# Performance work log

Measured on AMD Instinct MI355X. Metric: run time of the kernel, lower is better.

## Reference

```python
import jax, jax.numpy as jnp
import numpy as np
from math import sqrt

B, T, C, H = 4, 2048, 1024, 16
D = C // H  # head dim = 64


def setup_inputs() -> dict:
    key = jax.random.key(0)
    ks = jax.random.split(key, 9)
    s = 1.0 / sqrt(C)
    return {
        "x": jax.random.normal(ks[0], (B, T, C), dtype=jnp.float32),
        "Wk": jax.random.normal(ks[1], (C, C), dtype=jnp.float32) * s,
        "bk": jax.random.normal(ks[2], (C,), dtype=jnp.float32) * 0.01,
        "Wq": jax.random.normal(ks[3], (C, C), dtype=jnp.float32) * s,
        "bq": jax.random.normal(ks[4], (C,), dtype=jnp.float32) * 0.01,
        "Wv": jax.random.normal(ks[5], (C, C), dtype=jnp.float32) * s,
        "bv": jax.random.normal(ks[6], (C,), dtype=jnp.float32) * 0.01,
        "Wp": jax.random.normal(ks[7], (C, C), dtype=jnp.float32) * s,
        "bp": jax.random.normal(ks[8], (C,), dtype=jnp.float32) * 0.01,
    }


def reference(x, Wk, bk, Wq, bq, Wv, bv, Wp, bp):
    # Linear projections, split into heads: [B, H, T, D]
    def heads(y):
        return y.reshape(B, T, H, D).transpose(0, 2, 1, 3)

    k = heads(x @ Wk + bk)
    q = heads(x @ Wq + bq)
    v = heads(x @ Wv + bv)

    # scaled dot-product attention with causal mask (dropout p=0 -> identity)
    attn = jnp.einsum("bhtd,bhsd->bhts", q, k) / jnp.sqrt(jnp.float32(D))
    causal = jnp.tril(jnp.ones((T, T), dtype=bool))
    attn = jnp.where(causal[None, None], attn, -jnp.inf)
    attn = jax.nn.softmax(attn, axis=-1)

    y = jnp.einsum("bhts,bhsd->bhtd", attn, v)  # [B, H, T, D]
    y = y.transpose(0, 2, 1, 3).reshape(B, T, C)
    return y @ Wp + bp
```

## Files before the change

kernel.cpp:

```cpp
#include <hip/hip_runtime.h>
#include <hip/hip_bf16.h>
#include <math.h>


typedef short bf16x8 __attribute__((ext_vector_type(8)));
typedef float f32x4 __attribute__((ext_vector_type(4)));
typedef _Float16 f16x4 __attribute__((ext_vector_type(4)));

__device__ __forceinline__ short f2b(float f) {
    unsigned u = __float_as_uint(f);
    u = (u + 0x7fffu + ((u >> 16) & 1u)) >> 16;
    return (short)u;
}
__device__ __forceinline__ float b2f(short s) {
    return __uint_as_float(((unsigned)(unsigned short)s) << 16);
}

__global__ __launch_bounds__(256) void cast_x_kernel(const float* __restrict__ x,
                                                     short* __restrict__ xb, int n4) {
    int idx = blockIdx.x * 256 + threadIdx.x;
    if (idx >= n4) return;
    float4 v = ((const float4*)x)[idx];
    short4 o;
    o.x = f2b(v.x); o.y = f2b(v.y); o.z = f2b(v.z); o.w = f2b(v.w);
    ((short4*)xb)[idx] = o;
}

__global__ __launch_bounds__(256) void wtrans_kernel(const float* W0, const float* W1,
                                                     const float* W2, const float* W3,
                                                     short* O0, short* O1, short* O2, short* O3) {
    const float* W; short* O;
    switch (blockIdx.z) {
        case 0: W = W0; O = O0; break;
        case 1: W = W1; O = O1; break;
        case 2: W = W2; O = O2; break;
        default: W = W3; O = O3; break;
    }
    __shared__ __align__(16) float Ls[64 * 68];
    int tid = threadIdx.x;
    int n0 = blockIdx.x * 64, k0 = blockIdx.y * 64;
    #pragma unroll
    for (int it = 0; it < 4; ++it) {
        int c = tid + it * 256;
        int r = c >> 4, off = (c & 15) * 4;
        *(float4*)&Ls[r * 68 + off] = *(const float4*)&W[(k0 + r) * 1024 + n0 + off];
    }
    __syncthreads();
    #pragma unroll
    for (int it = 0; it < 2; ++it) {
        int c = tid + it * 256;
        int n = c >> 3, koff = (c & 7) * 8;
        union { short s[8]; int4 v; } u;
        #pragma unroll
        for (int k = 0; k < 8; ++k) u.s[k] = f2b(Ls[(koff + k) * 68 + n]);
        *(int4*)&O[(n0 + n) * 1024 + k0 + koff] = u.v;
    }
}

template<int MODE>
__global__ __launch_bounds__(512, 2) void gemm8_kernel(const short* __restrict__ A,
                                                       const short* Bt0, const short* Bt1, const short* Bt2,
                                                       const float* b0, const float* b1, const float* b2,
                                                       float s0, float s1, float s2,
                                                       void* O0, void* O1, void* O2) {
    int z = blockIdx.z;
    const short* Bt   = (z == 0) ? Bt0 : (z == 1) ? Bt1 : Bt2;
    const float* bias = (z == 0) ? b0  : (z == 1) ? b1  : b2;
    float scl         = (z == 0) ? s0  : (z == 1) ? s1  : s2;
    void* Out         = (z == 0) ? O0  : (z == 1) ? O1  : O2;

    __shared__ __align__(16) short lds[73728];

    int tid = threadIdx.x;
    int w = tid >> 6, lane = tid & 63, quad = lane >> 4, l15 = lane & 15;
    int m0 = blockIdx.x * 128, n0 = blockIdx.y * 256;

    int srccol = ((lane & 3) * 8) ^ ((lane & 32) ? 16 : 0);
    const short* pA0 = A  + (m0 + w * 16 + (lane >> 2)) * 1024 + srccol;
    const short* pA1 = pA0 + 32;
    const short* pB0 = Bt + (n0 + (2 * w) * 16 + (lane >> 2)) * 1024 + srccol;
    const short* pB1 = pB0 + 32;
    const short* pB2 = pB0 + 16 * 1024;
    const short* pB3 = pB2 + 32;

    int dA = (w * 2) * 512;
    int dB = 24576 + (w * 4) * 512;

    int offR = l15 * 64 + ((quad * 16) ^ ((l15 & 8) << 2));
    int ma4 = (w >> 2) * 4;
    int nb2 = (w & 3) * 2;
    int jrow0 = nb2, jrow1 = nb2 + 1, jrow2 = nb2 + 8, jrow3 = nb2 + 9;
    const char* ldsb = (const char*)lds;

    f32x4 acc[4][4] = {};

    bf16x8 afA[4], bfA[4], afB[4], bfB[4];

#define STG(p, off) __builtin_amdgcn_global_load_lds( \
        (const __attribute__((address_space(1))) unsigned int*)(p), \
        (__attribute__((address_space(3))) unsigned int*)&lds[off], 16, 0, 0)
#define RD(base, row, kk) (*(const bf16x8*)(ldsb + (base) + ((row) * 2 + (kk)) * 1024 + offR))

    STG(pA0,      dA);                 STG(pA1,      dA + 512);
    STG(pB0,      dB);                 STG(pB1,      dB + 512);
    STG(pB2,      dB + 1024);          STG(pB3,      dB + 1536);
    STG(pA0 + 64, 8192 + dA);          STG(pA1 + 64, 8192 + dA + 512);
    STG(pB0 + 64, 16384 + dB);         STG(pB1 + 64, 16384 + dB + 512);
    STG(pB2 + 64, 16384 + dB + 1024);  STG(pB3 + 64, 16384 + dB + 1536);
    asm volatile("s_waitcnt vmcnt(6)" ::: "memory");
    __builtin_amdgcn_s_barrier();
    __builtin_amdgcn_sched_barrier(0);

    #pragma unroll
    for (int i = 0; i < 4; ++i) afA[i] = RD(0, ma4 + i, 0);
    bfA[0] = RD(49152, jrow0, 0); bfA[1] = RD(49152, jrow1, 0);
    bfA[2] = RD(49152, jrow2, 0); bfA[3] = RD(49152, jrow3, 0);

    #pragma unroll
    for (int t = 0; t < 16; ++t) {
        const int rs  = t % 3;
        const int rs1 = (t + 1) % 3;
        const int ss  = (t + 2) % 3;
        const int Ar  = rs * 16384;
        const int Br  = 49152 + rs * 32768;
        const int Ar1 = rs1 * 16384;
        const int Br1 = 49152 + rs1 * 32768;

        #pragma unroll
        for (int i = 0; i < 4; ++i) afB[i] = RD(Ar, ma4 + i, 1);
        bfB[0] = RD(Br, jrow0, 1); bfB[1] = RD(Br, jrow1, 1);
        bfB[2] = RD(Br, jrow2, 1); bfB[3] = RD(Br, jrow3, 1);
        if (t + 2 < 16) {
            STG(pA0 + (t + 2) * 64, ss * 8192 + dA);
            STG(pA1 + (t + 2) * 64, ss * 8192 + dA + 512);
            STG(pB0 + (t + 2) * 64, ss * 16384 + dB);
        }
        asm volatile("s_waitcnt lgkmcnt(8)" ::: "memory");
        __builtin_amdgcn_sched_barrier(0);
        __builtin_amdgcn_s_setprio(1);
        #pragma unroll
        for (int i = 0; i < 4; ++i)
            #pragma unroll
            for (int j = 0; j < 4; ++j)
                acc[i][j] = __builtin_amdgcn_mfma_f32_16x16x32_bf16(afA[i], bfA[j], acc[i][j], 0, 0, 0);
        __builtin_amdgcn_s_setprio(0);
        if (t < 14) {
            asm volatile("s_waitcnt vmcnt(3)" ::: "memory");
        } else if (t == 14) {
            asm volatile("s_waitcnt vmcnt(0)" ::: "memory");
        }
        __builtin_amdgcn_s_barrier();
        __builtin_amdgcn_sched_barrier(0);

        if (t < 15) {
            #pragma unroll
            for (int i = 0; i < 4; ++i) afA[i] = RD(Ar1, ma4 + i, 0);
            bfA[0] = RD(Br1, jrow0, 0); bfA[1] = RD(Br1, jrow1, 0);
            bfA[2] = RD(Br1, jrow2, 0); bfA[3] = RD(Br1, jrow3, 0);
        }
        if (t + 2 < 16) {
            STG(pB1 + (t + 2) * 64, ss * 16384 + dB + 512);
            STG(pB2 + (t + 2) * 64, ss * 16384 + dB + 1024);
            STG(pB3 + (t + 2) * 64, ss * 16384 + dB + 1536);
        }
        if (t < 15) {
            asm volatile("s_waitcnt lgkmcnt(8)" ::: "memory");
        } else {
            asm volatile("s_waitcnt lgkmcnt(0)" ::: "memory");
        }
        __builtin_amdgcn_sched_barrier(0);
        __builtin_amdgcn_s_setprio(1);
        #pragma unroll
        for (int i = 0; i < 4; ++i)
            #pragma unroll
            for (int j = 0; j < 4; ++j)
                acc[i][j] = __builtin_amdgcn_mfma_f32_16x16x32_bf16(afB[i], bfB[j], acc[i][j], 0, 0, 0);
        __builtin_amdgcn_s_setprio(0);
        if (t < 15) {
            __builtin_amdgcn_s_barrier();
            __builtin_amdgcn_sched_barrier(0);
        }
    }
#undef STG
#undef RD

    int mrow = m0 + (w >> 2) * 64;
    int ncol = n0 + (w & 3) * 32;
    #pragma unroll
    for (int i = 0; i < 4; ++i) {
        #pragma unroll
        for (int j = 0; j < 4; ++j) {
            int gn = ncol + (j >> 1) * 128 + (j & 1) * 16 + l15;
            float bv = bias[gn];
            #pragma unroll
            for (int r = 0; r < 4; ++r) {
                int gm = mrow + i * 16 + quad * 4 + r;
                float v = (acc[i][j][r] + bv) * scl;
                if (MODE == 0) {
                    int b = gm >> 11, tt = gm & 2047, h = gn >> 6, d = gn & 63;
                    ((short*)Out)[(((b * 16 + h) * 2048) + tt) * 64 + d] = f2b(v);
                } else {
                    ((float*)Out)[gm * 1024 + gn] = v;
                }
            }
        }
    }
}

__global__ __launch_bounds__(256) void vtrans_kernel(const short* __restrict__ V,
                                                     _Float16* __restrict__ Vt) {
    __shared__ __align__(16) short Ts[64 * 72];
    int tid = threadIdx.x;
    int bh = blockIdx.y;
    int t0 = blockIdx.x * 64;
    #pragma unroll
    for (int it = 0; it < 2; ++it) {
        int c = tid + it * 256;
        int r = c >> 3, off = (c & 7) * 8;
        *(int4*)&Ts[r * 72 + off] = *(const int4*)&V[(bh * 2048 + t0 + r) * 64 + off];
    }
    __syncthreads();
    #pragma unroll
    for (int it = 0; it < 2; ++it) {
        int c = tid + it * 256;
        int d = c >> 3, toff = (c & 7) * 8;
        union { _Float16 h[8]; int4 v; } u;
        #pragma unroll
        for (int k = 0; k < 8; ++k) u.h[k] = (_Float16)b2f(Ts[(toff + k) * 72 + d]);
        *(int4*)&Vt[(bh * 64 + d) * 2048 + t0 + toff] = u.v;
    }
}

__global__ __launch_bounds__(256, 3) void attn_kernel(const short* __restrict__ Q,
                                                      const short* __restrict__ K,
                                                      const _Float16* __restrict__ Vt,
                                                      short* __restrict__ Y) {
    __shared__ __align__(16) short    Ks[128 * 64];
    __shared__ __align__(16) _Float16 Vs[64 * 128];

    int tid = threadIdx.x;
    int w = tid >> 6, lane = tid & 63, quad = lane >> 4, l15 = lane & 15;
    int idx = blockIdx.x;
    int qi = 15 - (idx >> 6);
    int bh = idx & 63;

    const short* Qh = Q + bh * 2048 * 64;
    const short* Kh = K + bh * 2048 * 64;
    const _Float16* Vh = Vt + bh * 64 * 2048;

    bf16x8 qf[2][2];
    #pragma unroll
    for (int i = 0; i < 2; ++i)
        #pragma unroll
        for (int kh = 0; kh < 2; ++kh) {
            int t = qi * 128 + w * 32 + i * 16 + l15;
            qf[i][kh] = *(const bf16x8*)&Qh[t * 64 + kh * 32 + quad * 8];
        }

    int krow = lane >> 3;
    int kchunk = ((lane & 7) ^ krow) * 8;
    int vrow = lane >> 4;
    int vchunk = ((lane & 15) ^ (w * 4 + vrow)) * 8;

    int t7 = l15 & 7;
    int kf0_off = ((quad ^ t7) * 8);
    int kf1_off = (((quad + 4) ^ t7) * 8);
    int vsub = (quad & 1) * 4;
    int vchi = quad >> 1;

    f32x4 o[2][4] = {};
    float lsum[2] = {0.f, 0.f};

    for (int si = 0; si <= qi; ++si) {
        const short* Kt = Kh + si * 128 * 64;
        const _Float16* Vtile = Vh + si * 128;
        bool diag = (si == qi);

        __syncthreads();
        #pragma unroll
        for (int it = 0; it < 4; ++it) {
            int kr0 = it * 32 + w * 8;
            __builtin_amdgcn_global_load_lds(
                (const __attribute__((address_space(1))) unsigned int*)&Kt[(kr0 + krow) * 64 + kchunk],
                (__attribute__((address_space(3))) unsigned int*)&Ks[kr0 * 64], 16, 0, 0);
            int vr0 = it * 16 + w * 4;
            __builtin_amdgcn_global_load_lds(
                (const __attribute__((address_space(1))) unsigned int*)&Vtile[(vr0 + vrow) * 2048 + vchunk],
                (__attribute__((address_space(3))) unsigned int*)&Vs[vr0 * 128], 16, 0, 0);
        }
        __syncthreads();

        #pragma unroll
        for (int j = 0; j < 8; ++j) {
            int trow = (j * 16 + l15) * 64;
            bf16x8 kf0 = *(const bf16x8*)&Ks[trow + kf0_off];
            bf16x8 kf1 = *(const bf16x8*)&Ks[trow + kf1_off];
            f16x4 pfv[2];
            #pragma unroll
            for (int i = 0; i < 2; ++i) {
                f32x4 a = {};
                a = __builtin_amdgcn_mfma_f32_16x16x32_bf16(kf0, qf[i][0], a, 0, 0, 0);
                a = __builtin_amdgcn_mfma_f32_16x16x32_bf16(kf1, qf[i][1], a, 0, 0, 0);
                if (diag) {
                    int qrel = w * 32 + i * 16 + l15;
                    #pragma unroll
                    for (int r = 0; r < 4; ++r)
                        if (j * 16 + quad * 4 + r > qrel) a[r] = -1e30f;
                }
                float p0 = __builtin_amdgcn_exp2f(a[0]);
                float p1 = __builtin_amdgcn_exp2f(a[1]);
                float p2 = __builtin_amdgcn_exp2f(a[2]);
                float p3 = __builtin_amdgcn_exp2f(a[3]);
                lsum[i] += (p0 + p1) + (p2 + p3);
                pfv[i][0] = (_Float16)p0;
                pfv[i][1] = (_Float16)p1;
                pfv[i][2] = (_Float16)p2;
                pfv[i][3] = (_Float16)p3;
            }
            int vc = (j * 2 + vchi);
            #pragma unroll
            for (int mt = 0; mt < 4; ++mt) {
                int d = mt * 16 + l15;
                f16x4 vf = *(const f16x4*)&Vs[d * 128 + ((vc ^ l15) * 8) + vsub];
                o[0][mt] = __builtin_amdgcn_mfma_f32_16x16x16f16(vf, pfv[0], o[0][mt], 0, 0, 0);
                o[1][mt] = __builtin_amdgcn_mfma_f32_16x16x16f16(vf, pfv[1], o[1][mt], 0, 0, 0);
            }
        }
    }

    int b = bh >> 4, h = bh & 15;
    #pragma unroll
    for (int i = 0; i < 2; ++i) {
        float l = lsum[i];
        l += __shfl_xor(l, 16);
        l += __shfl_xor(l, 32);
        float rinv = 1.0f / l;
        int q = qi * 128 + w * 32 + i * 16 + l15;
        short* yrow = &Y[(b * 2048 + q) * 1024 + h * 64];
        #pragma unroll
        for (int mt = 0; mt < 4; ++mt) {
            short4 s4;
            s4.x = f2b(o[i][mt][0] * rinv);
            s4.y = f2b(o[i][mt][1] * rinv);
            s4.z = f2b(o[i][mt][2] * rinv);
            s4.w = f2b(o[i][mt][3] * rinv);
            *(short4*)&yrow[mt * 16 + quad * 4] = s4;
        }
    }
}

extern "C" void kernel_launch(void* const* d_in, const int* in_sizes, int n_in,
                              void* d_out, int out_size, void* d_ws, size_t ws_size,
                              hipStream_t stream) {
    const float* x  = (const float*)d_in[0];
    const float* Wk = (const float*)d_in[1];
    const float* bk = (const float*)d_in[2];
    const float* Wq = (const float*)d_in[3];
    const float* bq = (const float*)d_in[4];
    const float* Wv = (const float*)d_in[5];
    const float* bv = (const float*)d_in[6];
    const float* Wp = (const float*)d_in[7];
    const float* bp = (const float*)d_in[8];

    char* ws = (char*)d_ws;
    short*     xb  = (short*)(ws + 0);
    short*     Wqt = (short*)(ws + 16777216);
    short*     Wkt = (short*)(ws + 18874368);
    short*     Wvt = (short*)(ws + 20971520);
    short*     Wpt = (short*)(ws + 23068672);
    short*     Qb  = (short*)(ws + 25165824);
    short*     Kb  = (short*)(ws + 41943040);
    short*     Vb  = (short*)(ws + 58720256);
    _Float16*  Vtb = (_Float16*)(ws + 75497472);
    short*     Yb  = (short*)(ws + 92274688);

    cast_x_kernel<<<8192, 256, 0, stream>>>(x, xb, 2097152);
    wtrans_kernel<<<dim3(16, 16, 4), 256, 0, stream>>>(Wq, Wk, Wv, Wp, Wqt, Wkt, Wvt, Wpt);
    gemm8_kernel<0><<<dim3(64, 4, 3), 512, 0, stream>>>(xb, Wqt, Wkt, Wvt, bq, bk, bv,
                                                        0.18033688011112042f , 1.0f, 1.0f,
                                                        (void*)Qb, (void*)Kb, (void*)Vb);
    vtrans_kernel<<<dim3(32, 64), 256, 0, stream>>>(Vb, Vtb);
    attn_kernel<<<1024, 256, 0, stream>>>(Qb, Kb, Vtb, Yb);
    gemm8_kernel<1><<<dim3(64, 4, 1), 512, 0, stream>>>(Yb, Wpt, nullptr, nullptr,
                                                        bp, nullptr, nullptr,
                                                        1.0f, 1.0f, 1.0f,
                                                        (void*)d_out, nullptr, nullptr);
}
```

Before: 242.5 us.

## Fuse V transpose into QKV GEMM epilogue and deepen LDS fragment prefetch

The QKV GEMM epilogue now writes V directly in transposed fp16 layout for the attention kernel, which removes the separate vtrans kernel launch and its extra read/write of V. The GEMM main loop is also restructured to keep three register fragment sets so LDS reads for the next half-step are issued while the current MFMAs run. In exchange, the global waits become stricter (vmcnt(0) before each barrier), which may expose load latency. Register pressure also rises from the extra fragment sets, and the fp16 store pattern in the epilogue is strided.

```diff
diff --git a/kernel.cpp b/kernel.cpp
--- a/kernel.cpp
+++ b/kernel.cpp
@@ -94,12 +94,31 @@
 
     f32x4 acc[4][4] = {};
 
-    bf16x8 afA[4], bfA[4], afB[4], bfB[4];
+    bf16x8 SA[3][4], SB[3][4];
 
 #define STG(p, off) __builtin_amdgcn_global_load_lds( \
         (const __attribute__((address_space(1))) unsigned int*)(p), \
         (__attribute__((address_space(3))) unsigned int*)&lds[off], 16, 0, 0)
 #define RD(base, row, kk) (*(const bf16x8*)(ldsb + (base) + ((row) * 2 + (kk)) * 1024 + offR))
+#define ISSUE_SET(s, TT, kk) do { \
+        const int _Ab = ((TT) % 3) * 16384; \
+        const int _Bb = 49152 + ((TT) % 3) * 32768; \
+        SA[s][0] = RD(_Ab, ma4 + 0, kk); \
+        SA[s][1] = RD(_Ab, ma4 + 1, kk); \
+        SA[s][2] = RD(_Ab, ma4 + 2, kk); \
+        SA[s][3] = RD(_Ab, ma4 + 3, kk); \
+        SB[s][0] = RD(_Bb, jrow0, kk); \
+        SB[s][1] = RD(_Bb, jrow1, kk); \
+        SB[s][2] = RD(_Bb, jrow2, kk); \
+        SB[s][3] = RD(_Bb, jrow3, kk); \
+    } while (0)
+#define MFMA_SET(s) do { \
+        _Pragma("unroll") \
+        for (int i = 0; i < 4; ++i) \
+            _Pragma("unroll") \
+            for (int j = 0; j < 4; ++j) \
+                acc[i][j] = __builtin_amdgcn_mfma_f32_16x16x32_bf16(SA[s][i], SB[s][j], acc[i][j], 0, 0, 0); \
+    } while (0)
 
     STG(pA0,      dA);                 STG(pA1,      dA + 512);
     STG(pB0,      dB);                 STG(pB1,      dB + 512);
@@ -107,82 +126,61 @@
     STG(pA0 + 64, 8192 + dA);          STG(pA1 + 64, 8192 + dA + 512);
     STG(pB0 + 64, 16384 + dB);         STG(pB1 + 64, 16384 + dB + 512);
     STG(pB2 + 64, 16384 + dB + 1024);  STG(pB3 + 64, 16384 + dB + 1536);
-    asm volatile("s_waitcnt vmcnt(6)" ::: "memory");
+    asm volatile("s_waitcnt vmcnt(0)" ::: "memory");
     __builtin_amdgcn_s_barrier();
     __builtin_amdgcn_sched_barrier(0);
 
-    #pragma unroll
-    for (int i = 0; i < 4; ++i) afA[i] = RD(0, ma4 + i, 0);
-    bfA[0] = RD(49152, jrow0, 0); bfA[1] = RD(49152, jrow1, 0);
-    bfA[2] = RD(49152, jrow2, 0); bfA[3] = RD(49152, jrow3, 0);
+    ISSUE_SET(0, 0, 0);
+    ISSUE_SET(1, 0, 1);
 
     #pragma unroll
     for (int t = 0; t < 16; ++t) {
-        const int rs  = t % 3;
-        const int rs1 = (t + 1) % 3;
+        const int s0  = (2 * t)     % 3;
+        const int s1  = (2 * t + 1) % 3;
+        const int sn0 = (2 * t + 2) % 3;
+        const int sn1 = (2 * t)     % 3;
         const int ss  = (t + 2) % 3;
-        const int Ar  = rs * 16384;
-        const int Br  = 49152 + rs * 32768;
-        const int Ar1 = rs1 * 16384;
-        const int Br1 = 49152 + rs1 * 32768;
-
-        #pragma unroll
-        for (int i = 0; i < 4; ++i) afB[i] = RD(Ar, ma4 + i, 1);
-        bfB[0] = RD(Br, jrow0, 1); bfB[1] = RD(Br, jrow1, 1);
-        bfB[2] = RD(Br, jrow2, 1); bfB[3] = RD(Br, jrow3, 1);
+
         if (t + 2 < 16) {
             STG(pA0 + (t + 2) * 64, ss * 8192 + dA);
             STG(pA1 + (t + 2) * 64, ss * 8192 + dA + 512);
             STG(pB0 + (t + 2) * 64, ss * 16384 + dB);
-        }
-        asm volatile("s_waitcnt lgkmcnt(8)" ::: "memory");
-        __builtin_amdgcn_sched_barrier(0);
-        __builtin_amdgcn_s_setprio(1);
-        #pragma unroll
-        for (int i = 0; i < 4; ++i)
-            #pragma unroll
-            for (int j = 0; j < 4; ++j)
-                acc[i][j] = __builtin_amdgcn_mfma_f32_16x16x32_bf16(afA[i], bfA[j], acc[i][j], 0, 0, 0);
-        __builtin_amdgcn_s_setprio(0);
-        if (t < 14) {
-            asm volatile("s_waitcnt vmcnt(3)" ::: "memory");
-        } else if (t == 14) {
-            asm volatile("s_waitcnt vmcnt(0)" ::: "memory");
-        }
-        __builtin_amdgcn_s_barrier();
-        __builtin_amdgcn_sched_barrier(0);
-
-        if (t < 15) {
-            #pragma unroll
-            for (int i = 0; i < 4; ++i) afA[i] = RD(Ar1, ma4 + i, 0);
-            bfA[0] = RD(Br1, jrow0, 0); bfA[1] = RD(Br1, jrow1, 0);
-            bfA[2] = RD(Br1, jrow2, 0); bfA[3] = RD(Br1, jrow3, 0);
-        }
-        if (t + 2 < 16) {
             STG(pB1 + (t + 2) * 64, ss * 16384 + dB + 512);
             STG(pB2 + (t + 2) * 64, ss * 16384 + dB + 1024);
             STG(pB3 + (t + 2) * 64, ss * 16384 + dB + 1536);
         }
-        if (t < 15) {
+        if (t + 1 < 16) {
+            ISSUE_SET(sn0, t + 1, 0);
+            asm volatile("s_waitcnt lgkmcnt(15)" ::: "memory");
+        } else {
             asm volatile("s_waitcnt lgkmcnt(8)" ::: "memory");
+        }
+        __builtin_amdgcn_sched_barrier(0);
+        __builtin_amdgcn_s_setprio(1);
+        MFMA_SET(s0);
+        __builtin_amdgcn_s_setprio(0);
+
+        if (t + 1 < 16) {
+            ISSUE_SET(sn1, t + 1, 1);
+            asm volatile("s_waitcnt lgkmcnt(15)" ::: "memory");
         } else {
             asm volatile("s_waitcnt lgkmcnt(0)" ::: "memory");
         }
         __builtin_amdgcn_sched_barrier(0);
         __builtin_amdgcn_s_setprio(1);
-        #pragma unroll
-        for (int i = 0; i < 4; ++i)
-            #pragma unroll
-            for (int j = 0; j < 4; ++j)
-                acc[i][j] = __builtin_amdgcn_mfma_f32_16x16x32_bf16(afB[i], bfB[j], acc[i][j], 0, 0, 0);
+        MFMA_SET(s1);
         __builtin_amdgcn_s_setprio(0);
+
         if (t < 15) {
+            asm volatile("s_waitcnt vmcnt(0)" ::: "memory");
             __builtin_amdgcn_s_barrier();
             __builtin_amdgcn_sched_barrier(0);
         }
     }
 #undef STG
 #undef RD
+#undef ISSUE_SET
+#undef MFMA_SET
 
     int mrow = m0 + (w >> 2) * 64;
     int ncol = n0 + (w & 3) * 32;
@@ -192,42 +190,27 @@
         for (int j = 0; j < 4; ++j) {
             int gn = ncol + (j >> 1) * 128 + (j & 1) * 16 + l15;
             float bv = bias[gn];
-            #pragma unroll
-            for (int r = 0; r < 4; ++r) {
-                int gm = mrow + i * 16 + quad * 4 + r;
-                float v = (acc[i][j][r] + bv) * scl;
-                if (MODE == 0) {
-                    int b = gm >> 11, tt = gm & 2047, h = gn >> 6, d = gn & 63;
-                    ((short*)Out)[(((b * 16 + h) * 2048) + tt) * 64 + d] = f2b(v);
-                } else {
-                    ((float*)Out)[gm * 1024 + gn] = v;
+            if (MODE == 0 && z == 2) {
+                int gm0 = mrow + i * 16 + quad * 4;
+                int b = gm0 >> 11, tt = gm0 & 2047, h = gn >> 6, d = gn & 63;
+                f16x4 hv;
+                #pragma unroll
+                for (int r = 0; r < 4; ++r) hv[r] = (_Float16)((acc[i][j][r] + bv) * scl);
+                *(f16x4*)&((_Float16*)Out)[((b * 16 + h) * 64 + d) * 2048 + tt] = hv;
+            } else {
+                #pragma unroll
+                for (int r = 0; r < 4; ++r) {
+                    int gm = mrow + i * 16 + quad * 4 + r;
+                    float v = (acc[i][j][r] + bv) * scl;
+                    if (MODE == 0) {
+                        int b = gm >> 11, tt = gm & 2047, h = gn >> 6, d = gn & 63;
+                        ((short*)Out)[(((b * 16 + h) * 2048) + tt) * 64 + d] = f2b(v);
+                    } else {
+                        ((float*)Out)[gm * 1024 + gn] = v;
+                    }
                 }
             }
         }
-    }
-}
-
-__global__ __launch_bounds__(256) void vtrans_kernel(const short* __restrict__ V,
-                                                     _Float16* __restrict__ Vt) {
-    __shared__ __align__(16) short Ts[64 * 72];
-    int tid = threadIdx.x;
-    int bh = blockIdx.y;
-    int t0 = blockIdx.x * 64;
-    #pragma unroll
-    for (int it = 0; it < 2; ++it) {
-        int c = tid + it * 256;
-        int r = c >> 3, off = (c & 7) * 8;
-        *(int4*)&Ts[r * 72 + off] = *(const int4*)&V[(bh * 2048 + t0 + r) * 64 + off];
-    }
-    __syncthreads();
-    #pragma unroll
-    for (int it = 0; it < 2; ++it) {
-        int c = tid + it * 256;
-        int d = c >> 3, toff = (c & 7) * 8;
-        union { _Float16 h[8]; int4 v; } u;
-        #pragma unroll
-        for (int k = 0; k < 8; ++k) u.h[k] = (_Float16)b2f(Ts[(toff + k) * 72 + d]);
-        *(int4*)&Vt[(bh * 64 + d) * 2048 + t0 + toff] = u.v;
     }
 }
 
@@ -370,7 +353,6 @@
     short*     Wpt = (short*)(ws + 23068672);
     short*     Qb  = (short*)(ws + 25165824);
     short*     Kb  = (short*)(ws + 41943040);
-    short*     Vb  = (short*)(ws + 58720256);
     _Float16*  Vtb = (_Float16*)(ws + 75497472);
     short*     Yb  = (short*)(ws + 92274688);
 
@@ -378,8 +360,7 @@
     wtrans_kernel<<<dim3(16, 16, 4), 256, 0, stream>>>(Wq, Wk, Wv, Wp, Wqt, Wkt, Wvt, Wpt);
     gemm8_kernel<0><<<dim3(64, 4, 3), 512, 0, stream>>>(xb, Wqt, Wkt, Wvt, bq, bk, bv,
                                                         0.18033688011112042f , 1.0f, 1.0f,
-                                                        (void*)Qb, (void*)Kb, (void*)Vb);
-    vtrans_kernel<<<dim3(32, 64), 256, 0, stream>>>(Vb, Vtb);
+                                                        (void*)Qb, (void*)Kb, (void*)Vtb);
     attn_kernel<<<1024, 256, 0, stream>>>(Qb, Kb, Vtb, Yb);
     gemm8_kernel<1><<<dim3(64, 4, 1), 512, 0, stream>>>(Yb, Wpt, nullptr, nullptr,
                                                         bp, nullptr, nullptr,
```

New measurement: 239.2 us. No clear change (-1.4%).

## Use 256x256-tile QKV GEMM with fused fp16 transposed V epilogue

Applied to the files above, without the earlier changes.

Adds a new QKV projection GEMM kernel that uses 256x256 output tiles per 512-thread block. It triple-buffers A and double-buffers B in LDS, with barrier and priority-staged MFMA phases. Its epilogue writes V directly in the transposed fp16 layout the attention kernel expects, so the separate vtrans kernel and the intermediate V buffer are removed. The larger tiles raise operand reuse, but they also raise LDS use and register pressure and halve the grid to 384 blocks, which may hurt occupancy.

```diff
diff --git a/kernel.cpp b/kernel.cpp
--- a/kernel.cpp
+++ b/kernel.cpp
@@ -54,6 +54,170 @@
         #pragma unroll
         for (int k = 0; k < 8; ++k) u.s[k] = f2b(Ls[(koff + k) * 68 + n]);
         *(int4*)&O[(n0 + n) * 1024 + k0 + koff] = u.v;
+    }
+}
+
+__global__ __launch_bounds__(512, 2) void gemm256_kernel(const short* __restrict__ A,
+                                                         const short* Bt0, const short* Bt1, const short* Bt2,
+                                                         const float* b0, const float* b1, const float* b2,
+                                                         float s0, float s1, float s2,
+                                                         void* O0, void* O1, void* O2) {
+    int z = blockIdx.z;
+    const short* Bt   = (z == 0) ? Bt0 : (z == 1) ? Bt1 : Bt2;
+    const float* bias = (z == 0) ? b0  : (z == 1) ? b1  : b2;
+    float scl         = (z == 0) ? s0  : (z == 1) ? s1  : s2;
+    void* Out         = (z == 0) ? O0  : (z == 1) ? O1  : O2;
+
+    __shared__ __align__(16) short lds[81920];
+
+    int tid = threadIdx.x;
+    int w = tid >> 6, lane = tid & 63, quad = lane >> 4, l15 = lane & 15;
+    int m0 = blockIdx.x * 256, n0 = blockIdx.y * 256;
+
+    int srccol = ((lane & 3) * 8) ^ ((lane & 32) ? 16 : 0);
+    const short* pA_w = A  + (m0 + (2 * w) * 16 + (lane >> 2)) * 1024 + srccol;
+    const short* pB_w = Bt + (n0 + (2 * w) * 16 + (lane >> 2)) * 1024 + srccol;
+    int dst_w = (2 * w) * 1024;
+
+    int offR = l15 * 64 + ((quad * 16) ^ ((l15 & 8) << 2));
+    int ar0 = (w >> 2) * 8;
+    int br0 = (w & 3) * 4;
+    const char* ldsb = (const char*)lds;
+
+    f32x4 acc[8][4] = {};
+    bf16x8 aF[4], bF[4];
+
+#define STG(p, off) __builtin_amdgcn_global_load_lds( \
+        (const __attribute__((address_space(1))) unsigned int*)(p), \
+        (__attribute__((address_space(3))) unsigned int*)&lds[off], 16, 0, 0)
+#define RDA(bb, r16, kk) (*(const bf16x8*)(ldsb + (bb) + ((r16) * 2 + (kk)) * 1024 + offR))
+#define RDB(bb, r16, kk) (*(const bf16x8*)(ldsb + 98304 + (bb) + ((r16) * 2 + (kk)) * 1024 + offR))
+#define PRE_MFMA do { __builtin_amdgcn_s_barrier(); \
+        asm volatile("s_waitcnt lgkmcnt(0)" ::: "memory"); \
+        __builtin_amdgcn_sched_barrier(0); \
+        __builtin_amdgcn_s_setprio(1); } while (0)
+#define POST_MFMA do { __builtin_amdgcn_s_setprio(0); \
+        __builtin_amdgcn_s_barrier(); \
+        __builtin_amdgcn_sched_barrier(0); } while (0)
+
+    STG(pA_w,                 dst_w);            STG(pA_w + 32,            dst_w + 512);
+    STG(pA_w + 16384,         dst_w + 1024);     STG(pA_w + 16384 + 32,    dst_w + 1536);
+    STG(pB_w,         49152 + dst_w);            STG(pB_w + 32,    49152 + dst_w + 512);
+    STG(pB_w + 16384, 49152 + dst_w + 1024);     STG(pB_w + 16384 + 32, 49152 + dst_w + 1536);
+    STG(pA_w + 64,            16384 + dst_w);        STG(pA_w + 96,            16384 + dst_w + 512);
+    STG(pA_w + 16384 + 64,    16384 + dst_w + 1024); STG(pA_w + 16384 + 96,    16384 + dst_w + 1536);
+    STG(pB_w + 64,    49152 + 16384 + dst_w);        STG(pB_w + 96,    49152 + 16384 + dst_w + 512);
+    STG(pB_w + 16384 + 64, 49152 + 16384 + dst_w + 1024);
+    STG(pB_w + 16384 + 96, 49152 + 16384 + dst_w + 1536);
+    asm volatile("s_waitcnt vmcnt(8)" ::: "memory");
+    __builtin_amdgcn_s_barrier();
+    __builtin_amdgcn_sched_barrier(0);
+
+    int aB0 = 0, aB1 = 32768, aB2 = 65536;
+    int bB0 = 0;
+    const short* sA = pA_w + 128;
+    const short* sB = pB_w + 64;
+
+    #pragma unroll 1
+    for (int t = 0; t < 16; ++t) {
+        int bN = 49152 + ((bB0 ^ 32768) >> 1) + dst_w;
+        int aN = (aB2 >> 1) + dst_w;
+
+        #pragma unroll
+        for (int i = 0; i < 4; ++i) aF[i] = RDA(aB0, ar0 + i, 0);
+        #pragma unroll
+        for (int j = 0; j < 4; ++j) bF[j] = RDB(bB0, br0 + j, 0);
+        if (t >= 1 && t < 15) { STG(sB, bN); STG(sB + 32, bN + 512); }
+        PRE_MFMA;
+        #pragma unroll
+        for (int i = 0; i < 4; ++i)
+            #pragma unroll
+            for (int j = 0; j < 4; ++j)
+                acc[i][j] = __builtin_amdgcn_mfma_f32_16x16x32_bf16(aF[i], bF[j], acc[i][j], 0, 0, 0);
+        POST_MFMA;
+
+        #pragma unroll
+        for (int i = 0; i < 4; ++i) aF[i] = RDA(aB0, ar0 + 4 + i, 0);
+        if (t >= 1 && t < 15) { STG(sB + 16384, bN + 1024); STG(sB + 16384 + 32, bN + 1536); }
+        PRE_MFMA;
+        #pragma unroll
+        for (int i = 0; i < 4; ++i)
+            #pragma unroll
+            for (int j = 0; j < 4; ++j)
+                acc[4 + i][j] = __builtin_amdgcn_mfma_f32_16x16x32_bf16(aF[i], bF[j], acc[4 + i][j], 0, 0, 0);
+        POST_MFMA;
+
+        #pragma unroll
+        for (int i = 0; i < 4; ++i) aF[i] = RDA(aB0, ar0 + i, 1);
+        #pragma unroll
+        for (int j = 0; j < 4; ++j) bF[j] = RDB(bB0, br0 + j, 1);
+        if (t < 14) { STG(sA, aN); STG(sA + 32, aN + 512); }
+        PRE_MFMA;
+        #pragma unroll
+        for (int i = 0; i < 4; ++i)
+            #pragma unroll
+            for (int j = 0; j < 4; ++j)
+                acc[i][j] = __builtin_amdgcn_mfma_f32_16x16x32_bf16(aF[i], bF[j], acc[i][j], 0, 0, 0);
+        POST_MFMA;
+
+        #pragma unroll
+        for (int i = 0; i < 4; ++i) aF[i] = RDA(aB0, ar0 + 4 + i, 1);
+        if (t < 14) { STG(sA + 16384, aN + 1024); STG(sA + 16384 + 32, aN + 1536); }
+        __builtin_amdgcn_s_barrier();
+        asm volatile("s_waitcnt lgkmcnt(0)" ::: "memory");
+        __builtin_amdgcn_sched_barrier(0);
+        __builtin_amdgcn_s_setprio(1);
+        #pragma unroll
+        for (int i = 0; i < 4; ++i)
+            #pragma unroll
+            for (int j = 0; j < 4; ++j)
+                acc[4 + i][j] = __builtin_amdgcn_mfma_f32_16x16x32_bf16(aF[i], bF[j], acc[4 + i][j], 0, 0, 0);
+        __builtin_amdgcn_s_setprio(0);
+        if (t < 14) {
+            asm volatile("s_waitcnt vmcnt(4)" ::: "memory");
+        } else if (t == 14) {
+            asm volatile("s_waitcnt vmcnt(0)" ::: "memory");
+        }
+        if (t < 15) {
+            __builtin_amdgcn_s_barrier();
+            __builtin_amdgcn_sched_barrier(0);
+        }
+
+        int tmp = aB0; aB0 = aB1; aB1 = aB2; aB2 = tmp;
+        bB0 ^= 32768;
+        sA += 64; sB += 64;
+    }
+#undef STG
+#undef RDA
+#undef RDB
+#undef PRE_MFMA
+#undef POST_MFMA
+
+    int mrow = m0 + (w >> 2) * 128;
+    int ncol = n0 + (w & 3) * 64;
+    #pragma unroll
+    for (int i = 0; i < 8; ++i) {
+        #pragma unroll
+        for (int j = 0; j < 4; ++j) {
+            int gn = ncol + j * 16 + l15;
+            float bv = bias[gn];
+            if (z == 2) {
+                int gm0 = mrow + i * 16 + quad * 4;
+                int b = gm0 >> 11, tt = gm0 & 2047, h = gn >> 6, d = gn & 63;
+                f16x4 hv;
+                #pragma unroll
+                for (int r = 0; r < 4; ++r) hv[r] = (_Float16)((acc[i][j][r] + bv) * scl);
+                *(f16x4*)&((_Float16*)Out)[((b * 16 + h) * 64 + d) * 2048 + tt] = hv;
+            } else {
+                #pragma unroll
+                for (int r = 0; r < 4; ++r) {
+                    int gm = mrow + i * 16 + quad * 4 + r;
+                    float v = (acc[i][j][r] + bv) * scl;
+                    int b = gm >> 11, tt = gm & 2047, h = gn >> 6, d = gn & 63;
+                    ((short*)Out)[(((b * 16 + h) * 2048) + tt) * 64 + d] = f2b(v);
+                }
+            }
+        }
     }
 }
 
@@ -93,7 +257,6 @@
     const char* ldsb = (const char*)lds;
 
     f32x4 acc[4][4] = {};
-
     bf16x8 afA[4], bfA[4], afB[4], bfB[4];
 
 #define STG(p, off) __builtin_amdgcn_global_load_lds( \
@@ -204,30 +367,6 @@
                 }
             }
         }
-    }
-}
-
-__global__ __launch_bounds__(256) void vtrans_kernel(const short* __restrict__ V,
-                                                     _Float16* __restrict__ Vt) {
-    __shared__ __align__(16) short Ts[64 * 72];
-    int tid = threadIdx.x;
-    int bh = blockIdx.y;
-    int t0 = blockIdx.x * 64;
-    #pragma unroll
-    for (int it = 0; it < 2; ++it) {
-        int c = tid + it * 256;
-        int r = c >> 3, off = (c & 7) * 8;
-        *(int4*)&Ts[r * 72 + off] = *(const int4*)&V[(bh * 2048 + t0 + r) * 64 + off];
-    }
-    __syncthreads();
-    #pragma unroll
-    for (int it = 0; it < 2; ++it) {
-        int c = tid + it * 256;
-        int d = c >> 3, toff = (c & 7) * 8;
-        union { _Float16 h[8]; int4 v; } u;
-        #pragma unroll
-        for (int k = 0; k < 8; ++k) u.h[k] = (_Float16)b2f(Ts[(toff + k) * 72 + d]);
-        *(int4*)&Vt[(bh * 64 + d) * 2048 + t0 + toff] = u.v;
     }
 }
 
@@ -370,16 +509,14 @@
     short*     Wpt = (short*)(ws + 23068672);
     short*     Qb  = (short*)(ws + 25165824);
     short*     Kb  = (short*)(ws + 41943040);
-    short*     Vb  = (short*)(ws + 58720256);
     _Float16*  Vtb = (_Float16*)(ws + 75497472);
     short*     Yb  = (short*)(ws + 92274688);
 
     cast_x_kernel<<<8192, 256, 0, stream>>>(x, xb, 2097152);
     wtrans_kernel<<<dim3(16, 16, 4), 256, 0, stream>>>(Wq, Wk, Wv, Wp, Wqt, Wkt, Wvt, Wpt);
-    gemm8_kernel<0><<<dim3(64, 4, 3), 512, 0, stream>>>(xb, Wqt, Wkt, Wvt, bq, bk, bv,
-                                                        0.18033688011112042f , 1.0f, 1.0f,
-                                                        (void*)Qb, (void*)Kb, (void*)Vb);
-    vtrans_kernel<<<dim3(32, 64), 256, 0, stream>>>(Vb, Vtb);
+    gemm256_kernel<<<dim3(32, 4, 3), 512, 0, stream>>>(xb, Wqt, Wkt, Wvt, bq, bk, bv,
+                                                       0.18033688011112042f , 1.0f, 1.0f,
+                                                       (void*)Qb, (void*)Kb, (void*)Vtb);
     attn_kernel<<<1024, 256, 0, stream>>>(Qb, Kb, Vtb, Yb);
     gemm8_kernel<1><<<dim3(64, 4, 1), 512, 0, stream>>>(Yb, Wpt, nullptr, nullptr,
                                                         bp, nullptr, nullptr,
```

New measurement: 252.2 us. 1.04x slower.

## Fuse V transpose into QKV GEMM epilogue and merge prep kernels

Applied to the files above, without the earlier changes.

The QKV GEMM epilogue for the V slice now writes fp16 directly in the transposed [bh, d, t] layout the attention kernel expects. This removes the separate vtrans kernel and its extra read/write of V. The x cast and weight-transpose kernels are also merged into one launch to save launch overhead. The transposed epilogue stores four contiguous fp16 values per lane with a 2048-element stride across lanes, so its global writes may be less coalesced.

```diff
diff --git a/kernel.cpp b/kernel.cpp
--- a/kernel.cpp
+++ b/kernel.cpp
@@ -16,29 +16,30 @@
     return __uint_as_float(((unsigned)(unsigned short)s) << 16);
 }
 
-__global__ __launch_bounds__(256) void cast_x_kernel(const float* __restrict__ x,
-                                                     short* __restrict__ xb, int n4) {
-    int idx = blockIdx.x * 256 + threadIdx.x;
-    if (idx >= n4) return;
-    float4 v = ((const float4*)x)[idx];
-    short4 o;
-    o.x = f2b(v.x); o.y = f2b(v.y); o.z = f2b(v.z); o.w = f2b(v.w);
-    ((short4*)xb)[idx] = o;
-}
-
-__global__ __launch_bounds__(256) void wtrans_kernel(const float* W0, const float* W1,
-                                                     const float* W2, const float* W3,
-                                                     short* O0, short* O1, short* O2, short* O3) {
+__global__ __launch_bounds__(256) void prep_kernel(const float* __restrict__ x, short* __restrict__ xb,
+                                                   const float* W0, const float* W1,
+                                                   const float* W2, const float* W3,
+                                                   short* O0, short* O1, short* O2, short* O3) {
+    int tid = threadIdx.x;
+    if (blockIdx.x < 8192) {
+        int idx = blockIdx.x * 256 + tid;
+        float4 v = ((const float4*)x)[idx];
+        short4 o;
+        o.x = f2b(v.x); o.y = f2b(v.y); o.z = f2b(v.z); o.w = f2b(v.w);
+        ((short4*)xb)[idx] = o;
+        return;
+    }
+    int wid = blockIdx.x - 8192;
     const float* W; short* O;
-    switch (blockIdx.z) {
+    switch (wid >> 8) {
         case 0: W = W0; O = O0; break;
         case 1: W = W1; O = O1; break;
         case 2: W = W2; O = O2; break;
         default: W = W3; O = O3; break;
     }
+    int rem = wid & 255;
+    int n0 = (rem >> 4) * 64, k0 = (rem & 15) * 64;
     __shared__ __align__(16) float Ls[64 * 68];
-    int tid = threadIdx.x;
-    int n0 = blockIdx.x * 64, k0 = blockIdx.y * 64;
     #pragma unroll
     for (int it = 0; it < 4; ++it) {
         int c = tid + it * 256;
@@ -93,7 +94,6 @@
     const char* ldsb = (const char*)lds;
 
     f32x4 acc[4][4] = {};
-
     bf16x8 afA[4], bfA[4], afB[4], bfB[4];
 
 #define STG(p, off) __builtin_amdgcn_global_load_lds( \
@@ -192,42 +192,27 @@
         for (int j = 0; j < 4; ++j) {
             int gn = ncol + (j >> 1) * 128 + (j & 1) * 16 + l15;
             float bv = bias[gn];
-            #pragma unroll
-            for (int r = 0; r < 4; ++r) {
-                int gm = mrow + i * 16 + quad * 4 + r;
-                float v = (acc[i][j][r] + bv) * scl;
-                if (MODE == 0) {
-                    int b = gm >> 11, tt = gm & 2047, h = gn >> 6, d = gn & 63;
-                    ((short*)Out)[(((b * 16 + h) * 2048) + tt) * 64 + d] = f2b(v);
-                } else {
-                    ((float*)Out)[gm * 1024 + gn] = v;
+            if (MODE == 0 && z == 2) {
+                int gm0 = mrow + i * 16 + quad * 4;
+                int b = gm0 >> 11, tt = gm0 & 2047, h = gn >> 6, d = gn & 63;
+                f16x4 hv;
+                #pragma unroll
+                for (int r = 0; r < 4; ++r) hv[r] = (_Float16)((acc[i][j][r] + bv) * scl);
+                *(f16x4*)&((_Float16*)Out)[((b * 16 + h) * 64 + d) * 2048 + tt] = hv;
+            } else {
+                #pragma unroll
+                for (int r = 0; r < 4; ++r) {
+                    int gm = mrow + i * 16 + quad * 4 + r;
+                    float v = (acc[i][j][r] + bv) * scl;
+                    if (MODE == 0) {
+                        int b = gm >> 11, tt = gm & 2047, h = gn >> 6, d = gn & 63;
+                        ((short*)Out)[(((b * 16 + h) * 2048) + tt) * 64 + d] = f2b(v);
+                    } else {
+                        ((float*)Out)[gm * 1024 + gn] = v;
+                    }
                 }
             }
         }
-    }
-}
-
-__global__ __launch_bounds__(256) void vtrans_kernel(const short* __restrict__ V,
-                                                     _Float16* __restrict__ Vt) {
-    __shared__ __align__(16) short Ts[64 * 72];
-    int tid = threadIdx.x;
-    int bh = blockIdx.y;
-    int t0 = blockIdx.x * 64;
-    #pragma unroll
-    for (int it = 0; it < 2; ++it) {
-        int c = tid + it * 256;
-        int r = c >> 3, off = (c & 7) * 8;
-        *(int4*)&Ts[r * 72 + off] = *(const int4*)&V[(bh * 2048 + t0 + r) * 64 + off];
-    }
-    __syncthreads();
-    #pragma unroll
-    for (int it = 0; it < 2; ++it) {
-        int c = tid + it * 256;
-        int d = c >> 3, toff = (c & 7) * 8;
-        union { _Float16 h[8]; int4 v; } u;
-        #pragma unroll
-        for (int k = 0; k < 8; ++k) u.h[k] = (_Float16)b2f(Ts[(toff + k) * 72 + d]);
-        *(int4*)&Vt[(bh * 64 + d) * 2048 + t0 + toff] = u.v;
     }
 }
 
@@ -370,16 +355,13 @@
     short*     Wpt = (short*)(ws + 23068672);
     short*     Qb  = (short*)(ws + 25165824);
     short*     Kb  = (short*)(ws + 41943040);
-    short*     Vb  = (short*)(ws + 58720256);
     _Float16*  Vtb = (_Float16*)(ws + 75497472);
     short*     Yb  = (short*)(ws + 92274688);
 
-    cast_x_kernel<<<8192, 256, 0, stream>>>(x, xb, 2097152);
-    wtrans_kernel<<<dim3(16, 16, 4), 256, 0, stream>>>(Wq, Wk, Wv, Wp, Wqt, Wkt, Wvt, Wpt);
+    prep_kernel<<<9216, 256, 0, stream>>>(x, xb, Wq, Wk, Wv, Wp, Wqt, Wkt, Wvt, Wpt);
     gemm8_kernel<0><<<dim3(64, 4, 3), 512, 0, stream>>>(xb, Wqt, Wkt, Wvt, bq, bk, bv,
                                                         0.18033688011112042f , 1.0f, 1.0f,
-                                                        (void*)Qb, (void*)Kb, (void*)Vb);
-    vtrans_kernel<<<dim3(32, 64), 256, 0, stream>>>(Vb, Vtb);
+                                                        (void*)Qb, (void*)Kb, (void*)Vtb);
     attn_kernel<<<1024, 256, 0, stream>>>(Qb, Kb, Vtb, Yb);
     gemm8_kernel<1><<<dim3(64, 4, 1), 512, 0, stream>>>(Yb, Wpt, nullptr, nullptr,
                                                         bp, nullptr, nullptr,
```

Measured after the change: 236.7 us. 1.02x faster.
